# Performance work log

Hardware: AMD Instinct MI355X
Metric: run time of the kernel (lower is better)

## Reference

```python
import jax, jax.numpy as jnp
import numpy as np

F = 128          # nbr_fea_len
A = 64           # angle_fea_len
N_EDGES = 100_000
N_ANGLES = 400_000
N_CRYST = 512
EPS = 1e-5
INV_SQRT_2 = 1.0 / 2.0 ** 0.5


def layer_norm(x, g, b):
    mu = jnp.mean(x, axis=-1, keepdims=True)
    var = jnp.var(x, axis=-1, keepdims=True)
    return (x - mu) * jax.lax.rsqrt(var + EPS) * g + b


def setup_inputs() -> dict:
    key = jax.random.key(0)
    ks = jax.random.split(key, 16)
    def lin(k, out_f, in_f):
        return (jax.random.normal(k, (out_f, in_f), jnp.float32) * (1.0 / np.sqrt(in_f))).astype(jnp.float32)
    return {
        "nbr_fea": jax.random.normal(ks[0], (N_EDGES, F), jnp.float32),
        "angle_fea": jax.random.normal(ks[1], (N_ANGLES, A), jnp.float32),
        "angle_nbr_idx": jax.random.randint(ks[2], (N_ANGLES, 2), 0, N_EDGES),
        "crystal_edge_idx": jax.random.randint(ks[3], (N_EDGES,), 0, N_CRYST),
        "crystal_angle_index": jnp.sort(jax.random.randint(ks[4], (N_ANGLES,), 0, N_CRYST)),
        "W_full": lin(ks[5], 2 * F, 2 * F + A),
        "W_mask": lin(ks[6], 1, F),
        "cn_gamma": jnp.ones((2 * F,), jnp.float32),
        "cn_beta": jnp.zeros((2 * F,), jnp.float32),
        "ln_core_g": jnp.ones((F,), jnp.float32),
        "ln_core_b": jnp.zeros((F,), jnp.float32),
        "ln2_g": jnp.ones((F,), jnp.float32),
        "ln2_b": jnp.zeros((F,), jnp.float32),
        "res_W1a": lin(ks[7], F // 2, F), "res_b1a": jnp.zeros((F // 2,), jnp.float32),
        "res_W2a": lin(ks[8], F, F // 2), "res_b2a": jnp.zeros((F,), jnp.float32),
        "res_W1b": lin(ks[9], F // 2, F), "res_b1b": jnp.zeros((F // 2,), jnp.float32),
        "res_W2b": lin(ks[10], F, F // 2), "res_b2b": jnp.zeros((F,), jnp.float32),
    }


def reference(nbr_fea, angle_fea, angle_nbr_idx, crystal_edge_idx, crystal_angle_index,
              W_full, W_mask, cn_gamma, cn_beta, ln_core_g, ln_core_b, ln2_g, ln2_b,
              res_W1a, res_b1a, res_W2a, res_b2a, res_W1b, res_b1b, res_W2b, res_b2b):
    source_idx = angle_nbr_idx[:, 0]
    # gather the two neighbor edge features per angle -> [n_angles, 2F]
    pair = nbr_fea[angle_nbr_idx].reshape(-1, 2 * F)
    total = jnp.concatenate([angle_fea, pair], axis=1)          # [n_angles, 2F+A]
    h = total @ W_full.T                                        # [n_angles, 2F]

    # Crystal_Norm: per-crystal, per-feature normalization over angle rows
    seg = crystal_angle_index
    cnt = jnp.maximum(jax.ops.segment_sum(jnp.ones((h.shape[0], 1), h.dtype), seg, N_CRYST), 1.0)
    mean = jax.ops.segment_sum(h, seg, N_CRYST) / cnt
    diff = h - mean[seg]
    var = jax.ops.segment_sum(diff * diff, seg, N_CRYST) / cnt
    h = diff * jax.lax.rsqrt(var + EPS)[seg] * cn_gamma + cn_beta

    nbr_core, nbr_filter = h[:, :F], h[:, F:]
    nbr_core = jax.nn.silu(layer_norm(nbr_core, ln_core_g, ln_core_b))
    gate = jax.nn.sigmoid(nbr_filter @ W_mask.T)                # [n_angles, 1]
    msg = gate * nbr_core

    # scatter-mean over source edge; empty edges get 0 (matches scatter+pad)
    s = jax.ops.segment_sum(msg, source_idx, N_EDGES)
    c = jax.ops.segment_sum(jnp.ones((msg.shape[0], 1), msg.dtype), source_idx, N_EDGES)
    nbr_sumed = s / jnp.maximum(c, 1.0)

    x = layer_norm(nbr_sumed, ln2_g, ln2_b)
    # two residual bottleneck blocks: x + fc2(silu(fc1(x)))
    x = x + (jax.nn.silu(x @ res_W1a.T + res_b1a) @ res_W2a.T + res_b2a)
    x = x + (jax.nn.silu(x @ res_W1b.T + res_b1b) @ res_W2b.T + res_b2b)
    return INV_SQRT_2 * (nbr_fea + x)
```

## Files before the change

kernel.cpp:

```cpp
#include <hip/hip_runtime.h>
#include <hip/hip_bf16.h>
#include <hip/hip_fp16.h>
#include <cstdint>
#include <cstddef>

#define NF 128
#define N_EDGES 100000
#define N_ANGLES 400000
#define N_CRYST 512
#define KDIM 320
#define TWOF 256
#define EPS_LN 1e-5f
#define INV_SQRT_2 0.70710678118654752440f
#define CAP 32

typedef short short8 __attribute__((ext_vector_type(8)));
typedef float floatx4 __attribute__((ext_vector_type(4)));

__device__ inline unsigned short f2bf(float x) {
    __hip_bfloat16 b = __float2bfloat16(x);
    return *reinterpret_cast<unsigned short*>(&b);
}
__device__ inline float bf2f(__hip_bfloat16 b) { return __bfloat162float(b); }
__device__ inline float bfbits2f(unsigned short u) {
    unsigned int v = ((unsigned int)u) << 16;
    return __uint_as_float(v);
}

__device__ inline uint4 cvt8(float4 a, float4 b) {
    __hip_bfloat162 p0 = __float22bfloat162_rn(make_float2(a.x, a.y));
    __hip_bfloat162 p1 = __float22bfloat162_rn(make_float2(a.z, a.w));
    __hip_bfloat162 p2 = __float22bfloat162_rn(make_float2(b.x, b.y));
    __hip_bfloat162 p3 = __float22bfloat162_rn(make_float2(b.z, b.w));
    uint4 r;
    r.x = *reinterpret_cast<unsigned int*>(&p0);
    r.y = *reinterpret_cast<unsigned int*>(&p1);
    r.z = *reinterpret_cast<unsigned int*>(&p2);
    r.w = *reinterpret_cast<unsigned int*>(&p3);
    return r;
}

__global__ void seg_bounds(const int* __restrict__ seg, int* __restrict__ seg_start) {
    int s = blockIdx.x * blockDim.x + threadIdx.x;
    if (s > N_CRYST) return;
    if (s == N_CRYST) { seg_start[N_CRYST] = N_ANGLES; return; }
    int lo = 0, hi = N_ANGLES;
    while (lo < hi) { int mid = (lo + hi) >> 1; if (seg[mid] < s) lo = mid + 1; else hi = mid; }
    seg_start[s] = lo;
}

__global__ __launch_bounds__(512) void gemm_gather_mfma(
    const float* __restrict__ angle_fea,
    const float* __restrict__ nbr_fea,
    const int*   __restrict__ angle_nbr_idx,
    const float* __restrict__ W_full,
    __hip_bfloat16* __restrict__ hout)
{
    __shared__ uint4 X_lds[512];
    __shared__ uint4 W_lds[1024];

    const int tid  = threadIdx.x;
    const int row0 = blockIdx.x * 128;

    const int xm = tid >> 2;
    const int xk = ((tid & 3) ^ ((xm >> 1) & 3)) * 8;
    const int p0 = angle_nbr_idx[(size_t)(row0 + xm) * 2 + 0];
    const int p1 = angle_nbr_idx[(size_t)(row0 + xm) * 2 + 1];
    int wn[2], wk[2];
    #pragma unroll
    for (int it = 0; it < 2; ++it) {
        int tau = it * 512 + tid;
        wn[it] = tau >> 2;
        wk[it] = ((tau & 3) ^ ((wn[it] >> 1) & 3)) * 8;
    }

    const int wave = tid >> 6, lane = tid & 63;
    const int wrow = (wave & 1) * 64;
    const int wcol = (wave >> 1) * 64;
    const int rl   = lane & 15, kgrp = lane >> 4;
    const int fragoff = (kgrp ^ ((rl >> 1) & 3)) * 16;
    const char* Xb = (const char*)X_lds;
    const char* Wb = (const char*)W_lds;

    floatx4 acc[4][4];
    #pragma unroll
    for (int i = 0; i < 4; ++i)
        #pragma unroll
        for (int j = 0; j < 4; ++j)
            acc[i][j] = (floatx4){0.f, 0.f, 0.f, 0.f};

    float4 xa, xb2, wa0, wb0, wa1, wb1;
    auto loadX = [&](int kbase, float4& a, float4& b) {
        const float* src;
        if (kbase < 64)       src = angle_fea + (size_t)(row0 + xm) * 64 + kbase + xk;
        else if (kbase < 192) src = nbr_fea + (size_t)p0 * 128 + (kbase - 64) + xk;
        else                  src = nbr_fea + (size_t)p1 * 128 + (kbase - 192) + xk;
        a = ((const float4*)src)[0];
        b = ((const float4*)src)[1];
    };
    auto loadW = [&](int kbase, int it, float4& a, float4& b) {
        const float* src = W_full + (size_t)wn[it] * KDIM + kbase + wk[it];
        a = ((const float4*)src)[0];
        b = ((const float4*)src)[1];
    };

    loadX(0, xa, xb2);
    loadW(0, 0, wa0, wb0);
    loadW(0, 1, wa1, wb1);

    #pragma unroll
    for (int kiter = 0; kiter < 10; ++kiter) {
        uint4 xc  = cvt8(xa, xb2);
        uint4 wc0 = cvt8(wa0, wb0);
        uint4 wc1 = cvt8(wa1, wb1);
        if (kiter > 0) __syncthreads();
        X_lds[tid]       = xc;
        W_lds[tid]       = wc0;
        W_lds[512 + tid] = wc1;
        __syncthreads();
        if (kiter < 9) {
            int nb = (kiter + 1) * 32;
            loadX(nb, xa, xb2);
            loadW(nb, 0, wa0, wb0);
            loadW(nb, 1, wa1, wb1);
        }
        short8 wf[4], xf[4];
        #pragma unroll
        for (int i = 0; i < 4; ++i)
            wf[i] = *(const short8*)(Wb + (size_t)(wcol + i * 16 + rl) * 64 + fragoff);
        #pragma unroll
        for (int j = 0; j < 4; ++j)
            xf[j] = *(const short8*)(Xb + (size_t)(wrow + j * 16 + rl) * 64 + fragoff);
        #pragma unroll
        for (int i = 0; i < 4; ++i)
            #pragma unroll
            for (int j = 0; j < 4; ++j)
                acc[i][j] = __builtin_amdgcn_mfma_f32_16x16x32_bf16(wf[i], xf[j], acc[i][j], 0, 0, 0);
    }

    unsigned short* hp = reinterpret_cast<unsigned short*>(hout);
    #pragma unroll
    for (int j = 0; j < 4; ++j) {
        size_t r = (size_t)(row0 + wrow + j * 16 + rl);
        #pragma unroll
        for (int i = 0; i < 4; ++i) {
            int c = wcol + i * 16 + kgrp * 4;
            floatx4 v = acc[i][j];
            uint2 pk;
            pk.x = (unsigned int)f2bf(v[0]) | ((unsigned int)f2bf(v[1]) << 16);
            pk.y = (unsigned int)f2bf(v[2]) | ((unsigned int)f2bf(v[3]) << 16);
            *reinterpret_cast<uint2*>(hp + r * TWOF + c) = pk;
        }
    }
}

__global__ __launch_bounds__(256) void seg_stats(
    const __hip_bfloat16* __restrict__ h,
    const int* __restrict__ seg_start,
    float* __restrict__ segSum, float* __restrict__ segSumSq)
{
    __shared__ float redS[8][256];
    __shared__ float redQ[8][256];
    int seg   = blockIdx.x;
    int split = blockIdx.y;
    int start = seg_start[seg], end = seg_start[seg + 1];
    int n = end - start;
    int g = threadIdx.x >> 5, t = threadIdx.x & 31;
    float s[8] = {0.f,0.f,0.f,0.f,0.f,0.f,0.f,0.f};
    float q[8] = {0.f,0.f,0.f,0.f,0.f,0.f,0.f,0.f};
    if (n > 0) {
        int per = (n + 3) >> 2;
        int r0 = start + split * per;
        int r1 = min(r0 + per, end);
        const unsigned short* hp = (const unsigned short*)h;
        for (int r = r0 + g; r < r1; r += 8) {
            uint4 v = *(const uint4*)(hp + (size_t)r * TWOF + t * 8);
            unsigned int d[4] = {v.x, v.y, v.z, v.w};
            #pragma unroll
            for (int i = 0; i < 4; ++i) {
                float lo = __uint_as_float(d[i] << 16);
                float hi = __uint_as_float(d[i] & 0xffff0000u);
                s[2*i]   += lo; q[2*i]   += lo * lo;
                s[2*i+1] += hi; q[2*i+1] += hi * hi;
            }
        }
    }
    #pragma unroll
    for (int i = 0; i < 8; ++i) { redS[g][t * 8 + i] = s[i]; redQ[g][t * 8 + i] = q[i]; }
    __syncthreads();
    if (n > 0) {
        int col = threadIdx.x;
        float S = 0.f, Q = 0.f;
        #pragma unroll
        for (int gg = 0; gg < 8; ++gg) { S += redS[gg][col]; Q += redQ[gg][col]; }
        atomicAdd(&segSum[seg * TWOF + col], S);
        atomicAdd(&segSumSq[seg * TWOF + col], Q);
    }
}

__global__ __launch_bounds__(256) void seg_finalize(
    const int* __restrict__ seg_start,
    float* __restrict__ segSum, float* __restrict__ segSumSq)
{
    int seg = blockIdx.x;
    int j = threadIdx.x;
    float cnt = (float)max(seg_start[seg + 1] - seg_start[seg], 1);
    float inv = 1.0f / cnt;
    float mean = segSum[seg * TWOF + j] * inv;
    float var  = segSumSq[seg * TWOF + j] * inv - mean * mean;
    segSum[seg * TWOF + j]   = mean;
    segSumSq[seg * TWOF + j] = rsqrtf(var + EPS_LN);
}

__global__ __launch_bounds__(256) void angle_msg(
    __hip_bfloat16* __restrict__ h,
    const int* __restrict__ seg_idx,
    const int* __restrict__ angle_nbr_idx,
    const float* __restrict__ segMean, const float* __restrict__ segScale,
    const float* __restrict__ cn_gamma, const float* __restrict__ cn_beta,
    const float* __restrict__ ln_g, const float* __restrict__ ln_b,
    const float* __restrict__ w_mask,
    int* __restrict__ slot_cnt, int* __restrict__ slots)
{
    int row  = blockIdx.x * 4 + (threadIdx.x >> 6);
    int lane = threadIdx.x & 63;
    int seg  = seg_idx[row];
    int src  = angle_nbr_idx[(size_t)row * 2];

    __hip_bfloat16* hr = h + (size_t)row * TWOF;
    float y[4];
    #pragma unroll
    for (int qq = 0; qq < 4; ++qq) {
        int col = lane + qq * 64;
        float v = bf2f(hr[col]);
        float m = segMean[seg * TWOF + col], sc = segScale[seg * TWOF + col];
        y[qq] = (v - m) * sc * cn_gamma[col] + cn_beta[col];
    }
    float sum = y[0] + y[1], ssq = y[0] * y[0] + y[1] * y[1];
    #pragma unroll
    for (int o = 32; o > 0; o >>= 1) { sum += __shfl_xor(sum, o, 64); ssq += __shfl_xor(ssq, o, 64); }
    float mu  = sum * (1.f / 128.f);
    float var = ssq * (1.f / 128.f) - mu * mu;
    float rs  = rsqrtf(var + EPS_LN);
    float ln0 = (y[0] - mu) * rs * ln_g[lane]      + ln_b[lane];
    float ln1 = (y[1] - mu) * rs * ln_g[lane + 64] + ln_b[lane + 64];
    float si0 = ln0 / (1.f + __expf(-ln0));
    float si1 = ln1 / (1.f + __expf(-ln1));
    float gp = y[2] * w_mask[lane] + y[3] * w_mask[lane + 64];
    #pragma unroll
    for (int o = 32; o > 0; o >>= 1) gp += __shfl_xor(gp, o, 64);
    float gate = 1.f / (1.f + __expf(-gp));

    __half* mrow = reinterpret_cast<__half*>(hr);
    mrow[lane]      = __float2half(gate * si0);
    mrow[lane + 64] = __float2half(gate * si1);

    if (lane == 0) {
        int k = atomicAdd(&slot_cnt[src], 1);
        if (k < CAP) slots[(size_t)src * CAP + k] = row;
    }
}

#define MT 64
#define XBS 136
#define H1S 72
#define W1S 136
#define W2S 72
__global__ __launch_bounds__(256) void edge_mlp_mfma(
    const __hip_bfloat16* __restrict__ hmsg,
    const int* __restrict__ slot_cnt,
    const int* __restrict__ slots,
    const float* __restrict__ nbr_fea,
    const float* __restrict__ ln2_g, const float* __restrict__ ln2_b,
    const float* __restrict__ W1a, const float* __restrict__ b1a,
    const float* __restrict__ W2a, const float* __restrict__ b2a,
    const float* __restrict__ W1b, const float* __restrict__ b1b,
    const float* __restrict__ W2b, const float* __restrict__ b2b,
    float* __restrict__ out)
{
    __shared__ unsigned short xb[MT * XBS];
    __shared__ unsigned short h1[MT * H1S];
    __shared__ unsigned short wl[128 * W2S];

    const int tid  = threadIdx.x;
    const int row0 = blockIdx.x * MT;
    const int w    = tid >> 6, lane = tid & 63;
    const int rl   = lane & 15, kgrp = lane >> 4;

    {
        int m = tid >> 2;
        int q = tid & 3;
        int e = min(row0 + m, N_EDGES - 1);
        int cnt = min(slot_cnt[e], CAP);
        float v[32];
        #pragma unroll
        for (int i = 0; i < 32; ++i) v[i] = 0.f;
        const char* hb = (const char*)hmsg;
        for (int k = 0; k < cnt; ++k) {
            int r = slots[(size_t)e * CAP + k];
            const uint4* mr = (const uint4*)(hb + (size_t)r * 512 + q * 64);
            #pragma unroll
            for (int t = 0; t < 4; ++t) {
                uint4 u = mr[t];
                unsigned int d[4] = {u.x, u.y, u.z, u.w};
                #pragma unroll
                for (int i2 = 0; i2 < 4; ++i2) {
                    __half2 hh = *reinterpret_cast<__half2*>(&d[i2]);
                    float2 f2 = __half22float2(hh);
                    v[8*t + 2*i2]     += f2.x;
                    v[8*t + 2*i2 + 1] += f2.y;
                }
            }
        }
        float inv = 1.f / fmaxf((float)cnt, 1.f);
        float sum = 0.f, ssq = 0.f;
        #pragma unroll
        for (int i = 0; i < 32; ++i) { v[i] *= inv; sum += v[i]; ssq += v[i] * v[i]; }
        sum += __shfl_xor(sum, 1, 64); ssq += __shfl_xor(ssq, 1, 64);
        sum += __shfl_xor(sum, 2, 64); ssq += __shfl_xor(ssq, 2, 64);
        float mu  = sum * (1.f / 128.f);
        float var = ssq * (1.f / 128.f) - mu * mu;
        float rs  = rsqrtf(var + EPS_LN);
        #pragma unroll
        for (int i = 0; i < 32; ++i) {
            int col = q * 32 + i;
            v[i] = (v[i] - mu) * rs * ln2_g[col] + ln2_b[col];
        }
        #pragma unroll
        for (int t = 0; t < 4; ++t) {
            float4 a = make_float4(v[8*t+0], v[8*t+1], v[8*t+2], v[8*t+3]);
            float4 b = make_float4(v[8*t+4], v[8*t+5], v[8*t+6], v[8*t+7]);
            *(uint4*)&xb[m * XBS + q * 32 + t * 8] = cvt8(a, b);
        }
    }

    const float* W1s[2] = {W1a, W1b};
    const float* B1s[2] = {b1a, b1b};
    const float* W2s[2] = {W2a, W2b};
    const float* B2s[2] = {b2a, b2b};

    #pragma unroll 1
    for (int blk = 0; blk < 2; ++blk) {
        const float* W1 = W1s[blk]; const float* B1 = B1s[blk];
        const float* W2 = W2s[blk]; const float* B2 = B2s[blk];

        __syncthreads();
        #pragma unroll
        for (int c = tid; c < 1024; c += 256) {
            int nn = c >> 4, kc = c & 15;
            const float* src = W1 + (size_t)nn * 128 + kc * 8;
            *(uint4*)&wl[nn * W1S + kc * 8] =
                cvt8(((const float4*)src)[0], ((const float4*)src)[1]);
        }
        __syncthreads();

        short8 xf[4];
        #pragma unroll
        for (int ks = 0; ks < 4; ++ks)
            xf[ks] = *(const short8*)&xb[(w * 16 + rl) * XBS + ks * 32 + kgrp * 8];
        floatx4 a1[4];
        #pragma unroll
        for (int i = 0; i < 4; ++i) {
            a1[i] = (floatx4){0.f, 0.f, 0.f, 0.f};
            #pragma unroll
            for (int ks = 0; ks < 4; ++ks) {
                short8 wf = *(const short8*)&wl[(i * 16 + rl) * W1S + ks * 32 + kgrp * 8];
                a1[i] = __builtin_amdgcn_mfma_f32_16x16x32_bf16(wf, xf[ks], a1[i], 0, 0, 0);
            }
        }
        #pragma unroll
        for (int i = 0; i < 4; ++i) {
            int nb = i * 16 + kgrp * 4;
            float s0 = a1[i][0] + B1[nb + 0];
            float s1 = a1[i][1] + B1[nb + 1];
            float s2 = a1[i][2] + B1[nb + 2];
            float s3 = a1[i][3] + B1[nb + 3];
            s0 = s0 / (1.f + __expf(-s0));
            s1 = s1 / (1.f + __expf(-s1));
            s2 = s2 / (1.f + __expf(-s2));
            s3 = s3 / (1.f + __expf(-s3));
            unsigned int lo = (unsigned int)f2bf(s0) | ((unsigned int)f2bf(s1) << 16);
            unsigned int hi = (unsigned int)f2bf(s2) | ((unsigned int)f2bf(s3) << 16);
            *(unsigned int*)&h1[(w * 16 + rl) * H1S + nb]     = lo;
            *(unsigned int*)&h1[(w * 16 + rl) * H1S + nb + 2] = hi;
        }

        __syncthreads();
        #pragma unroll
        for (int c = tid; c < 1024; c += 256) {
            int pp = c >> 3, kc = c & 7;
            const float* src = W2 + (size_t)pp * 64 + kc * 8;
            *(uint4*)&wl[pp * W2S + kc * 8] =
                cvt8(((const float4*)src)[0], ((const float4*)src)[1]);
        }
        __syncthreads();

        short8 hf[2];
        #pragma unroll
        for (int ks = 0; ks < 2; ++ks)
            hf[ks] = *(const short8*)&h1[(w * 16 + rl) * H1S + ks * 32 + kgrp * 8];
        #pragma unroll
        for (int p = 0; p < 8; ++p) {
            floatx4 a2 = (floatx4){0.f, 0.f, 0.f, 0.f};
            #pragma unroll
            for (int ks = 0; ks < 2; ++ks) {
                short8 wf = *(const short8*)&wl[(p * 16 + rl) * W2S + ks * 32 + kgrp * 8];
                a2 = __builtin_amdgcn_mfma_f32_16x16x32_bf16(wf, hf[ks], a2, 0, 0, 0);
            }
            int m = w * 16 + rl;
            #pragma unroll
            for (int reg = 0; reg < 4; ++reg) {
                int pcol = p * 16 + kgrp * 4 + reg;
                int idx  = m * XBS + pcol;
                float xv = bfbits2f(xb[idx]);
                xb[idx] = f2bf(xv + a2[reg] + B2[pcol]);
            }
        }
    }

    {
        int m = tid >> 2;
        int q = tid & 3;
        int e = row0 + m;
        if (e < N_EDGES) {
            const float4* nf = (const float4*)(nbr_fea + (size_t)e * NF + q * 32);
            float4* dst      = (float4*)(out + (size_t)e * NF + q * 32);
            #pragma unroll
            for (int t = 0; t < 8; ++t) {
                float4 f = nf[t];
                int col = q * 32 + 4 * t;
                dst[t] = make_float4(
                    INV_SQRT_2 * (f.x + bfbits2f(xb[m * XBS + col + 0])),
                    INV_SQRT_2 * (f.y + bfbits2f(xb[m * XBS + col + 1])),
                    INV_SQRT_2 * (f.z + bfbits2f(xb[m * XBS + col + 2])),
                    INV_SQRT_2 * (f.w + bfbits2f(xb[m * XBS + col + 3])));
            }
        }
    }
}


extern "C" void kernel_launch(void* const* d_in, const int* in_sizes, int n_in,
                              void* d_out, int out_size, void* d_ws, size_t ws_size,
                              hipStream_t stream) {
    const float* nbr_fea       = (const float*)d_in[0];
    const float* angle_fea     = (const float*)d_in[1];
    const int*   angle_nbr_idx = (const int*)d_in[2];
    const int*   cai           = (const int*)d_in[4];
    const float* W_full        = (const float*)d_in[5];
    const float* W_mask        = (const float*)d_in[6];
    const float* cn_gamma      = (const float*)d_in[7];
    const float* cn_beta       = (const float*)d_in[8];
    const float* ln_core_g     = (const float*)d_in[9];
    const float* ln_core_b     = (const float*)d_in[10];
    const float* ln2_g         = (const float*)d_in[11];
    const float* ln2_b         = (const float*)d_in[12];
    const float* W1a           = (const float*)d_in[13];
    const float* b1a           = (const float*)d_in[14];
    const float* W2a           = (const float*)d_in[15];
    const float* b2a           = (const float*)d_in[16];
    const float* W1b           = (const float*)d_in[17];
    const float* b1b           = (const float*)d_in[18];
    const float* W2b           = (const float*)d_in[19];
    const float* b2b           = (const float*)d_in[20];
    float* out = (float*)d_out;

    char* ws = (char*)d_ws;
    float* segSum    = (float*)(ws + 0);
    float* segSumSq  = (float*)(ws + 524288);
    int*   slot_cnt  = (int*)  (ws + 1048576);
    int*   seg_start = (int*)  (ws + 1448576);
    int*   slots     = (int*)  (ws + 1450752);
    __hip_bfloat16* h = (__hip_bfloat16*)(ws + 14250752);

    hipMemsetAsync(ws, 0, 1448576, stream);

    seg_bounds<<<3, 256, 0, stream>>>(cai, seg_start);
    gemm_gather_mfma<<<N_ANGLES / 128, 512, 0, stream>>>(
        angle_fea, nbr_fea, angle_nbr_idx, W_full, h);
    seg_stats<<<dim3(N_CRYST, 4), 256, 0, stream>>>(h, seg_start, segSum, segSumSq);
    seg_finalize<<<N_CRYST, 256, 0, stream>>>(seg_start, segSum, segSumSq);
    angle_msg<<<N_ANGLES / 4, 256, 0, stream>>>(
        h, cai, angle_nbr_idx, segSum, segSumSq,
        cn_gamma, cn_beta, ln_core_g, ln_core_b, W_mask, slot_cnt, slots);
    edge_mlp_mfma<<<(N_EDGES + MT - 1) / MT, 256, 0, stream>>>(
        h, slot_cnt, slots, nbr_fea, ln2_g, ln2_b,
        W1a, b1a, W2a, b2a, W1b, b1b, W2b, b2b, out);
}
```

Measured before the change: 666.1 us.

## Fuse segment statistics into GEMM epilogue and double-buffer GEMM LDS

After: 718.9 us. 1.08x slower.

```diff
diff --git a/kernel.cpp b/kernel.cpp
--- a/kernel.cpp
+++ b/kernel.cpp
@@ -54,10 +54,12 @@
     const float* __restrict__ nbr_fea,
     const int*   __restrict__ angle_nbr_idx,
     const float* __restrict__ W_full,
+    const int*   __restrict__ cai,
+    float* __restrict__ segSum, float* __restrict__ segSumSq,
     __hip_bfloat16* __restrict__ hout)
 {
-    __shared__ uint4 X_lds[512];
-    __shared__ uint4 W_lds[1024];
+    __shared__ uint4 X_lds[2][512];
+    __shared__ uint4 W_lds[2][1024];
 
     const int tid  = threadIdx.x;
     const int row0 = blockIdx.x * 128;
@@ -79,8 +81,6 @@
     const int wcol = (wave >> 1) * 64;
     const int rl   = lane & 15, kgrp = lane >> 4;
     const int fragoff = (kgrp ^ ((rl >> 1) & 3)) * 16;
-    const char* Xb = (const char*)X_lds;
-    const char* Wb = (const char*)W_lds;
 
     floatx4 acc[4][4];
     #pragma unroll
@@ -89,41 +89,44 @@
         for (int j = 0; j < 4; ++j)
             acc[i][j] = (floatx4){0.f, 0.f, 0.f, 0.f};
 
-    float4 xa, xb2, wa0, wb0, wa1, wb1;
-    auto loadX = [&](int kbase, float4& a, float4& b) {
+    float4 xr[2][2];
+    float4 wr[2][4];
+    auto loadX = [&](int kbase, int s) {
         const float* src;
         if (kbase < 64)       src = angle_fea + (size_t)(row0 + xm) * 64 + kbase + xk;
         else if (kbase < 192) src = nbr_fea + (size_t)p0 * 128 + (kbase - 64) + xk;
         else                  src = nbr_fea + (size_t)p1 * 128 + (kbase - 192) + xk;
-        a = ((const float4*)src)[0];
-        b = ((const float4*)src)[1];
+        xr[s][0] = ((const float4*)src)[0];
+        xr[s][1] = ((const float4*)src)[1];
     };
-    auto loadW = [&](int kbase, int it, float4& a, float4& b) {
-        const float* src = W_full + (size_t)wn[it] * KDIM + kbase + wk[it];
-        a = ((const float4*)src)[0];
-        b = ((const float4*)src)[1];
+    auto loadW = [&](int kbase, int s) {
+        const float* s0 = W_full + (size_t)wn[0] * KDIM + kbase + wk[0];
+        wr[s][0] = ((const float4*)s0)[0];
+        wr[s][1] = ((const float4*)s0)[1];
+        const float* s1 = W_full + (size_t)wn[1] * KDIM + kbase + wk[1];
+        wr[s][2] = ((const float4*)s1)[0];
+        wr[s][3] = ((const float4*)s1)[1];
     };
 
-    loadX(0, xa, xb2);
-    loadW(0, 0, wa0, wb0);
-    loadW(0, 1, wa1, wb1);
-
-    #pragma unroll
-    for (int kiter = 0; kiter < 10; ++kiter) {
-        uint4 xc  = cvt8(xa, xb2);
-        uint4 wc0 = cvt8(wa0, wb0);
-        uint4 wc1 = cvt8(wa1, wb1);
-        if (kiter > 0) __syncthreads();
-        X_lds[tid]       = xc;
-        W_lds[tid]       = wc0;
-        W_lds[512 + tid] = wc1;
-        __syncthreads();
-        if (kiter < 9) {
-            int nb = (kiter + 1) * 32;
-            loadX(nb, xa, xb2);
-            loadW(nb, 0, wa0, wb0);
-            loadW(nb, 1, wa1, wb1);
-        }
+    loadX(0, 0);  loadW(0, 0);
+    loadX(32, 1); loadW(32, 1);
+    {
+        uint4 xc  = cvt8(xr[0][0], xr[0][1]);
+        uint4 wc0 = cvt8(wr[0][0], wr[0][1]);
+        uint4 wc1 = cvt8(wr[0][2], wr[0][3]);
+        X_lds[0][tid]       = xc;
+        W_lds[0][tid]       = wc0;
+        W_lds[0][512 + tid] = wc1;
+    }
+    loadX(64, 0); loadW(64, 0);
+    asm volatile("s_waitcnt lgkmcnt(0)" ::: "memory");
+    __builtin_amdgcn_s_barrier();
+
+    #pragma unroll
+    for (int k = 0; k < 10; ++k) {
+        const int cur = k & 1, nxt = (k + 1) & 1;
+        const char* Xb = (const char*)X_lds[cur];
+        const char* Wb = (const char*)W_lds[cur];
         short8 wf[4], xf[4];
         #pragma unroll
         for (int i = 0; i < 4; ++i)
@@ -131,11 +134,27 @@
         #pragma unroll
         for (int j = 0; j < 4; ++j)
             xf[j] = *(const short8*)(Xb + (size_t)(wrow + j * 16 + rl) * 64 + fragoff);
+        if (k < 9) {
+            uint4 xc  = cvt8(xr[nxt][0], xr[nxt][1]);
+            uint4 wc0 = cvt8(wr[nxt][0], wr[nxt][1]);
+            uint4 wc1 = cvt8(wr[nxt][2], wr[nxt][3]);
+            X_lds[nxt][tid]       = xc;
+            W_lds[nxt][tid]       = wc0;
+            W_lds[nxt][512 + tid] = wc1;
+            if (k + 3 <= 9) {
+                loadX((k + 3) * 32, nxt);
+                loadW((k + 3) * 32, nxt);
+            }
+        }
         #pragma unroll
         for (int i = 0; i < 4; ++i)
             #pragma unroll
             for (int j = 0; j < 4; ++j)
                 acc[i][j] = __builtin_amdgcn_mfma_f32_16x16x32_bf16(wf[i], xf[j], acc[i][j], 0, 0, 0);
+        if (k < 9) {
+            asm volatile("s_waitcnt lgkmcnt(0)" ::: "memory");
+            __builtin_amdgcn_s_barrier();
+        }
     }
 
     unsigned short* hp = reinterpret_cast<unsigned short*>(hout);
@@ -152,49 +171,55 @@
             *reinterpret_cast<uint2*>(hp + r * TWOF + c) = pk;
         }
     }
-}
-
-__global__ __launch_bounds__(256) void seg_stats(
-    const __hip_bfloat16* __restrict__ h,
-    const int* __restrict__ seg_start,
-    float* __restrict__ segSum, float* __restrict__ segSumSq)
-{
-    __shared__ float redS[8][256];
-    __shared__ float redQ[8][256];
-    int seg   = blockIdx.x;
-    int split = blockIdx.y;
-    int start = seg_start[seg], end = seg_start[seg + 1];
-    int n = end - start;
-    int g = threadIdx.x >> 5, t = threadIdx.x & 31;
-    float s[8] = {0.f,0.f,0.f,0.f,0.f,0.f,0.f,0.f};
-    float q[8] = {0.f,0.f,0.f,0.f,0.f,0.f,0.f,0.f};
-    if (n > 0) {
-        int per = (n + 3) >> 2;
-        int r0 = start + split * per;
-        int r1 = min(r0 + per, end);
-        const unsigned short* hp = (const unsigned short*)h;
-        for (int r = r0 + g; r < r1; r += 8) {
-            uint4 v = *(const uint4*)(hp + (size_t)r * TWOF + t * 8);
-            unsigned int d[4] = {v.x, v.y, v.z, v.w};
-            #pragma unroll
-            for (int i = 0; i < 4; ++i) {
-                float lo = __uint_as_float(d[i] << 16);
-                float hi = __uint_as_float(d[i] & 0xffff0000u);
-                s[2*i]   += lo; q[2*i]   += lo * lo;
-                s[2*i+1] += hi; q[2*i+1] += hi * hi;
-            }
-        }
-    }
-    #pragma unroll
-    for (int i = 0; i < 8; ++i) { redS[g][t * 8 + i] = s[i]; redQ[g][t * 8 + i] = q[i]; }
-    __syncthreads();
-    if (n > 0) {
-        int col = threadIdx.x;
-        float S = 0.f, Q = 0.f;
-        #pragma unroll
-        for (int gg = 0; gg < 8; ++gg) { S += redS[gg][col]; Q += redQ[gg][col]; }
-        atomicAdd(&segSum[seg * TWOF + col], S);
-        atomicAdd(&segSumSq[seg * TWOF + col], Q);
+
+    float* red = (float*)&X_lds[0][0];
+    int sj[4];
+    #pragma unroll
+    for (int j = 0; j < 4; ++j) sj[j] = cai[row0 + wrow + j * 16 + rl];
+    const int sA = cai[row0], sB = cai[row0 + 127];
+    for (int s = sA; s <= sB; ++s) {
+        float S[16], Q[16];
+        #pragma unroll
+        for (int t = 0; t < 16; ++t) { S[t] = 0.f; Q[t] = 0.f; }
+        #pragma unroll
+        for (int j = 0; j < 4; ++j) {
+            float msk = (sj[j] == s) ? 1.f : 0.f;
+            #pragma unroll
+            for (int i = 0; i < 4; ++i)
+                #pragma unroll
+                for (int g = 0; g < 4; ++g) {
+                    float v = acc[i][j][g] * msk;
+                    S[i * 4 + g] += v;
+                    Q[i * 4 + g] += v * v;
+                }
+        }
+        #pragma unroll
+        for (int t = 0; t < 16; ++t) {
+            #pragma unroll
+            for (int d = 1; d < 16; d <<= 1) {
+                S[t] += __shfl_xor(S[t], d, 64);
+                Q[t] += __shfl_xor(Q[t], d, 64);
+            }
+        }
+        __syncthreads();
+        if (rl == 0) {
+            #pragma unroll
+            for (int i = 0; i < 4; ++i)
+                #pragma unroll
+                for (int g = 0; g < 4; ++g) {
+                    int col = wcol + i * 16 + kgrp * 4 + g;
+                    red[((wave & 1) * 256 + col) * 2 + 0] = S[i * 4 + g];
+                    red[((wave & 1) * 256 + col) * 2 + 1] = Q[i * 4 + g];
+                }
+        }
+        __syncthreads();
+        if (tid < 256) {
+            int col = tid;
+            float Ss = red[col * 2]     + red[(256 + col) * 2];
+            float Qs = red[col * 2 + 1] + red[(256 + col) * 2 + 1];
+            atomicAdd(&segSum[(size_t)s * TWOF + col], Ss);
+            atomicAdd(&segSumSq[(size_t)s * TWOF + col], Qs);
+        }
     }
 }
 
@@ -227,33 +252,45 @@
     int seg  = seg_idx[row];
     int src  = angle_nbr_idx[(size_t)row * 2];
 
-    __hip_bfloat16* hr = h + (size_t)row * TWOF;
-    float y[4];
-    #pragma unroll
-    for (int qq = 0; qq < 4; ++qq) {
-        int col = lane + qq * 64;
-        float v = bf2f(hr[col]);
-        float m = segMean[seg * TWOF + col], sc = segScale[seg * TWOF + col];
-        y[qq] = (v - m) * sc * cn_gamma[col] + cn_beta[col];
-    }
-    float sum = y[0] + y[1], ssq = y[0] * y[0] + y[1] * y[1];
+    unsigned short* hr = reinterpret_cast<unsigned short*>(h + (size_t)row * TWOF);
+    const int c0 = 2 * lane;
+    unsigned int ucore = ((const unsigned int*)hr)[lane];
+    unsigned int ufilt = ((const unsigned int*)hr)[lane + 64];
+
+    float2 m0 = *(const float2*)&segMean[seg * TWOF + c0];
+    float2 s0 = *(const float2*)&segScale[seg * TWOF + c0];
+    float2 m1 = *(const float2*)&segMean[seg * TWOF + 128 + c0];
+    float2 s1 = *(const float2*)&segScale[seg * TWOF + 128 + c0];
+    float2 g0 = *(const float2*)&cn_gamma[c0];
+    float2 b0 = *(const float2*)&cn_beta[c0];
+    float2 g1 = *(const float2*)&cn_gamma[128 + c0];
+    float2 b1 = *(const float2*)&cn_beta[128 + c0];
+
+    float y0 = (bfbits2f((unsigned short)(ucore & 0xffffu)) - m0.x) * s0.x * g0.x + b0.x;
+    float y1 = (bfbits2f((unsigned short)(ucore >> 16))     - m0.y) * s0.y * g0.y + b0.y;
+    float y2 = (bfbits2f((unsigned short)(ufilt & 0xffffu)) - m1.x) * s1.x * g1.x + b1.x;
+    float y3 = (bfbits2f((unsigned short)(ufilt >> 16))     - m1.y) * s1.y * g1.y + b1.y;
+
+    float sum = y0 + y1, ssq = y0 * y0 + y1 * y1;
     #pragma unroll
     for (int o = 32; o > 0; o >>= 1) { sum += __shfl_xor(sum, o, 64); ssq += __shfl_xor(ssq, o, 64); }
     float mu  = sum * (1.f / 128.f);
     float var = ssq * (1.f / 128.f) - mu * mu;
     float rs  = rsqrtf(var + EPS_LN);
-    float ln0 = (y[0] - mu) * rs * ln_g[lane]      + ln_b[lane];
-    float ln1 = (y[1] - mu) * rs * ln_g[lane + 64] + ln_b[lane + 64];
+    float2 lg = *(const float2*)&ln_g[c0];
+    float2 lb = *(const float2*)&ln_b[c0];
+    float ln0 = (y0 - mu) * rs * lg.x + lb.x;
+    float ln1 = (y1 - mu) * rs * lg.y + lb.y;
     float si0 = ln0 / (1.f + __expf(-ln0));
     float si1 = ln1 / (1.f + __expf(-ln1));
-    float gp = y[2] * w_mask[lane] + y[3] * w_mask[lane + 64];
+    float2 wm = *(const float2*)&w_mask[c0];
+    float gp = y2 * wm.x + y3 * wm.y;
     #pragma unroll
     for (int o = 32; o > 0; o >>= 1) gp += __shfl_xor(gp, o, 64);
     float gate = 1.f / (1.f + __expf(-gp));
 
-    __half* mrow = reinterpret_cast<__half*>(hr);
-    mrow[lane]      = __float2half(gate * si0);
-    mrow[lane + 64] = __float2half(gate * si1);
+    __half2 hh = __floats2half2_rn(gate * si0, gate * si1);
+    ((unsigned int*)hr)[lane] = *reinterpret_cast<unsigned int*>(&hh);
 
     if (lane == 0) {
         int k = atomicAdd(&slot_cnt[src], 1);
@@ -477,8 +514,7 @@
 
     seg_bounds<<<3, 256, 0, stream>>>(cai, seg_start);
     gemm_gather_mfma<<<N_ANGLES / 128, 512, 0, stream>>>(
-        angle_fea, nbr_fea, angle_nbr_idx, W_full, h);
-    seg_stats<<<dim3(N_CRYST, 4), 256, 0, stream>>>(h, seg_start, segSum, segSumSq);
+        angle_fea, nbr_fea, angle_nbr_idx, W_full, cai, segSum, segSumSq, h);
     seg_finalize<<<N_CRYST, 256, 0, stream>>>(seg_start, segSum, segSumSq);
     angle_msg<<<N_ANGLES / 4, 256, 0, stream>>>(
         h, cai, angle_nbr_idx, segSum, segSumSq,
```

## Fuse per-crystal sum and sum-of-squares into the gather GEMM epilogue

Applied to the files above, without the earlier changes.

After: 750.2 us. 12.6% more time.

```diff
diff --git a/kernel.cpp b/kernel.cpp
--- a/kernel.cpp
+++ b/kernel.cpp
@@ -54,10 +54,13 @@
     const float* __restrict__ nbr_fea,
     const int*   __restrict__ angle_nbr_idx,
     const float* __restrict__ W_full,
+    const int*   __restrict__ cai,
+    float* __restrict__ segSum, float* __restrict__ segSumSq,
     __hip_bfloat16* __restrict__ hout)
 {
     __shared__ uint4 X_lds[512];
     __shared__ uint4 W_lds[1024];
+    __shared__ float red[1024];
 
     const int tid  = threadIdx.x;
     const int row0 = blockIdx.x * 128;
@@ -152,49 +155,43 @@
             *reinterpret_cast<uint2*>(hp + r * TWOF + c) = pk;
         }
     }
-}
-
-__global__ __launch_bounds__(256) void seg_stats(
-    const __hip_bfloat16* __restrict__ h,
-    const int* __restrict__ seg_start,
-    float* __restrict__ segSum, float* __restrict__ segSumSq)
-{
-    __shared__ float redS[8][256];
-    __shared__ float redQ[8][256];
-    int seg   = blockIdx.x;
-    int split = blockIdx.y;
-    int start = seg_start[seg], end = seg_start[seg + 1];
-    int n = end - start;
-    int g = threadIdx.x >> 5, t = threadIdx.x & 31;
-    float s[8] = {0.f,0.f,0.f,0.f,0.f,0.f,0.f,0.f};
-    float q[8] = {0.f,0.f,0.f,0.f,0.f,0.f,0.f,0.f};
-    if (n > 0) {
-        int per = (n + 3) >> 2;
-        int r0 = start + split * per;
-        int r1 = min(r0 + per, end);
-        const unsigned short* hp = (const unsigned short*)h;
-        for (int r = r0 + g; r < r1; r += 8) {
-            uint4 v = *(const uint4*)(hp + (size_t)r * TWOF + t * 8);
-            unsigned int d[4] = {v.x, v.y, v.z, v.w};
-            #pragma unroll
-            for (int i = 0; i < 4; ++i) {
-                float lo = __uint_as_float(d[i] << 16);
-                float hi = __uint_as_float(d[i] & 0xffff0000u);
-                s[2*i]   += lo; q[2*i]   += lo * lo;
-                s[2*i+1] += hi; q[2*i+1] += hi * hi;
-            }
-        }
-    }
-    #pragma unroll
-    for (int i = 0; i < 8; ++i) { redS[g][t * 8 + i] = s[i]; redQ[g][t * 8 + i] = q[i]; }
-    __syncthreads();
-    if (n > 0) {
-        int col = threadIdx.x;
-        float S = 0.f, Q = 0.f;
-        #pragma unroll
-        for (int gg = 0; gg < 8; ++gg) { S += redS[gg][col]; Q += redQ[gg][col]; }
-        atomicAdd(&segSum[seg * TWOF + col], S);
-        atomicAdd(&segSumSq[seg * TWOF + col], Q);
+
+    int sj[4];
+    #pragma unroll
+    for (int j = 0; j < 4; ++j) sj[j] = cai[row0 + wrow + j * 16 + rl];
+    const int sA = cai[row0], sB = cai[row0 + 127];
+    for (int s = sA; s <= sB; ++s) {
+        __syncthreads();
+        #pragma unroll
+        for (int i = 0; i < 4; ++i) {
+            #pragma unroll
+            for (int g = 0; g < 4; ++g) {
+                float S = 0.f, Q = 0.f;
+                #pragma unroll
+                for (int j = 0; j < 4; ++j) {
+                    float v = (sj[j] == s) ? acc[i][j][g] : 0.f;
+                    S += v;
+                    Q += v * v;
+                }
+                S += __shfl_xor(S, 1, 64); Q += __shfl_xor(Q, 1, 64);
+                S += __shfl_xor(S, 2, 64); Q += __shfl_xor(Q, 2, 64);
+                S += __shfl_xor(S, 4, 64); Q += __shfl_xor(Q, 4, 64);
+                S += __shfl_xor(S, 8, 64); Q += __shfl_xor(Q, 8, 64);
+                if (rl == 0) {
+                    int col = wcol + i * 16 + kgrp * 4 + g;
+                    red[((wave & 1) * 256 + col) * 2 + 0] = S;
+                    red[((wave & 1) * 256 + col) * 2 + 1] = Q;
+                }
+            }
+        }
+        __syncthreads();
+        if (tid < 256) {
+            int col = tid;
+            float Ss = red[col * 2]     + red[(256 + col) * 2];
+            float Qs = red[col * 2 + 1] + red[(256 + col) * 2 + 1];
+            atomicAdd(&segSum[(size_t)s * TWOF + col], Ss);
+            atomicAdd(&segSumSq[(size_t)s * TWOF + col], Qs);
+        }
     }
 }
 
@@ -477,8 +474,7 @@
 
     seg_bounds<<<3, 256, 0, stream>>>(cai, seg_start);
     gemm_gather_mfma<<<N_ANGLES / 128, 512, 0, stream>>>(
-        angle_fea, nbr_fea, angle_nbr_idx, W_full, h);
-    seg_stats<<<dim3(N_CRYST, 4), 256, 0, stream>>>(h, seg_start, segSum, segSumSq);
+        angle_fea, nbr_fea, angle_nbr_idx, W_full, cai, segSum, segSumSq, h);
     seg_finalize<<<N_CRYST, 256, 0, stream>>>(seg_start, segSum, segSumSq);
     angle_msg<<<N_ANGLES / 4, 256, 0, stream>>>(
         h, cai, angle_nbr_idx, segSum, segSumSq,
```

## Fuse per-angle message computation into edge MLP gather, precompute affine norm

Applied to the files above, without the earlier changes.

Measured after the change: 826.2 us. +24.0%, slower.

```diff
diff --git a/kernel.cpp b/kernel.cpp
--- a/kernel.cpp
+++ b/kernel.cpp
@@ -47,6 +47,17 @@
     int lo = 0, hi = N_ANGLES;
     while (lo < hi) { int mid = (lo + hi) >> 1; if (seg[mid] < s) lo = mid + 1; else hi = mid; }
     seg_start[s] = lo;
+}
+
+__global__ __launch_bounds__(256) void slot_build(
+    const int* __restrict__ angle_nbr_idx,
+    int* __restrict__ slot_cnt, int* __restrict__ slots)
+{
+    int row = blockIdx.x * 256 + threadIdx.x;
+    if (row >= N_ANGLES) return;
+    int src = angle_nbr_idx[(size_t)row * 2];
+    int k = atomicAdd(&slot_cnt[src], 1);
+    if (k < CAP) slots[(size_t)src * CAP + k] = row;
 }
 
 __global__ __launch_bounds__(512) void gemm_gather_mfma(
@@ -200,6 +211,7 @@
 
 __global__ __launch_bounds__(256) void seg_finalize(
     const int* __restrict__ seg_start,
+    const float* __restrict__ cn_gamma, const float* __restrict__ cn_beta,
     float* __restrict__ segSum, float* __restrict__ segSumSq)
 {
     int seg = blockIdx.x;
@@ -208,57 +220,11 @@
     float inv = 1.0f / cnt;
     float mean = segSum[seg * TWOF + j] * inv;
     float var  = segSumSq[seg * TWOF + j] * inv - mean * mean;
-    segSum[seg * TWOF + j]   = mean;
-    segSumSq[seg * TWOF + j] = rsqrtf(var + EPS_LN);
-}
-
-__global__ __launch_bounds__(256) void angle_msg(
-    __hip_bfloat16* __restrict__ h,
-    const int* __restrict__ seg_idx,
-    const int* __restrict__ angle_nbr_idx,
-    const float* __restrict__ segMean, const float* __restrict__ segScale,
-    const float* __restrict__ cn_gamma, const float* __restrict__ cn_beta,
-    const float* __restrict__ ln_g, const float* __restrict__ ln_b,
-    const float* __restrict__ w_mask,
-    int* __restrict__ slot_cnt, int* __restrict__ slots)
-{
-    int row  = blockIdx.x * 4 + (threadIdx.x >> 6);
-    int lane = threadIdx.x & 63;
-    int seg  = seg_idx[row];
-    int src  = angle_nbr_idx[(size_t)row * 2];
-
-    __hip_bfloat16* hr = h + (size_t)row * TWOF;
-    float y[4];
-    #pragma unroll
-    for (int qq = 0; qq < 4; ++qq) {
-        int col = lane + qq * 64;
-        float v = bf2f(hr[col]);
-        float m = segMean[seg * TWOF + col], sc = segScale[seg * TWOF + col];
-        y[qq] = (v - m) * sc * cn_gamma[col] + cn_beta[col];
-    }
-    float sum = y[0] + y[1], ssq = y[0] * y[0] + y[1] * y[1];
-    #pragma unroll
-    for (int o = 32; o > 0; o >>= 1) { sum += __shfl_xor(sum, o, 64); ssq += __shfl_xor(ssq, o, 64); }
-    float mu  = sum * (1.f / 128.f);
-    float var = ssq * (1.f / 128.f) - mu * mu;
-    float rs  = rsqrtf(var + EPS_LN);
-    float ln0 = (y[0] - mu) * rs * ln_g[lane]      + ln_b[lane];
-    float ln1 = (y[1] - mu) * rs * ln_g[lane + 64] + ln_b[lane + 64];
-    float si0 = ln0 / (1.f + __expf(-ln0));
-    float si1 = ln1 / (1.f + __expf(-ln1));
-    float gp = y[2] * w_mask[lane] + y[3] * w_mask[lane + 64];
-    #pragma unroll
-    for (int o = 32; o > 0; o >>= 1) gp += __shfl_xor(gp, o, 64);
-    float gate = 1.f / (1.f + __expf(-gp));
-
-    __half* mrow = reinterpret_cast<__half*>(hr);
-    mrow[lane]      = __float2half(gate * si0);
-    mrow[lane + 64] = __float2half(gate * si1);
-
-    if (lane == 0) {
-        int k = atomicAdd(&slot_cnt[src], 1);
-        if (k < CAP) slots[(size_t)src * CAP + k] = row;
-    }
+    float rs   = rsqrtf(var + EPS_LN);
+    float A = rs * cn_gamma[j];
+    float B = cn_beta[j] - mean * A;
+    segSum[seg * TWOF + j]   = A;
+    segSumSq[seg * TWOF + j] = B;
 }
 
 #define MT 64
@@ -267,10 +233,14 @@
 #define W1S 136
 #define W2S 72
 __global__ __launch_bounds__(256) void edge_mlp_mfma(
-    const __hip_bfloat16* __restrict__ hmsg,
+    const __hip_bfloat16* __restrict__ h,
+    const int* __restrict__ cai,
     const int* __restrict__ slot_cnt,
     const int* __restrict__ slots,
+    const float* __restrict__ segA, const float* __restrict__ segB,
     const float* __restrict__ nbr_fea,
+    const float* __restrict__ lncg, const float* __restrict__ lncb,
+    const float* __restrict__ w_mask,
     const float* __restrict__ ln2_g, const float* __restrict__ ln2_b,
     const float* __restrict__ W1a, const float* __restrict__ b1a,
     const float* __restrict__ W2a, const float* __restrict__ b2a,
@@ -281,41 +251,100 @@
     __shared__ unsigned short xb[MT * XBS];
     __shared__ unsigned short h1[MT * H1S];
     __shared__ unsigned short wl[128 * W2S];
+    __shared__ float lnw[384];
 
     const int tid  = threadIdx.x;
     const int row0 = blockIdx.x * MT;
     const int w    = tid >> 6, lane = tid & 63;
     const int rl   = lane & 15, kgrp = lane >> 4;
+
+    if (tid < 128) {
+        lnw[tid]       = lncg[tid];
+        lnw[128 + tid] = lncb[tid];
+        lnw[256 + tid] = w_mask[tid];
+    }
+    __syncthreads();
 
     {
         int m = tid >> 2;
         int q = tid & 3;
         int e = min(row0 + m, N_EDGES - 1);
         int cnt = min(slot_cnt[e], CAP);
-        float v[32];
-        #pragma unroll
-        for (int i = 0; i < 32; ++i) v[i] = 0.f;
-        const char* hb = (const char*)hmsg;
+        float acc[32];
+        #pragma unroll
+        for (int i = 0; i < 32; ++i) acc[i] = 0.f;
+        const char* hb = (const char*)h;
+
         for (int k = 0; k < cnt; ++k) {
-            int r = slots[(size_t)e * CAP + k];
-            const uint4* mr = (const uint4*)(hb + (size_t)r * 512 + q * 64);
+            int r   = slots[(size_t)e * CAP + k];
+            int seg = cai[r];
+            const uint4* hrow = (const uint4*)(hb + (size_t)r * 512);
+            const float* Asg = segA + (size_t)seg * TWOF;
+            const float* Bsg = segB + (size_t)seg * TWOF;
+
+            float y[32];
+            float sum = 0.f, ssq = 0.f, gp = 0.f;
             #pragma unroll
             for (int t = 0; t < 4; ++t) {
-                uint4 u = mr[t];
-                unsigned int d[4] = {u.x, u.y, u.z, u.w};
+                uint4 u = hrow[q * 4 + t];
+                float A8[8], B8[8];
+                *(float4*)&A8[0] = *(const float4*)(Asg + q * 32 + t * 8);
+                *(float4*)&A8[4] = *(const float4*)(Asg + q * 32 + t * 8 + 4);
+                *(float4*)&B8[0] = *(const float4*)(Bsg + q * 32 + t * 8);
+                *(float4*)&B8[4] = *(const float4*)(Bsg + q * 32 + t * 8 + 4);
+                unsigned int dd[4] = {u.x, u.y, u.z, u.w};
                 #pragma unroll
-                for (int i2 = 0; i2 < 4; ++i2) {
-                    __half2 hh = *reinterpret_cast<__half2*>(&d[i2]);
-                    float2 f2 = __half22float2(hh);
-                    v[8*t + 2*i2]     += f2.x;
-                    v[8*t + 2*i2 + 1] += f2.y;
+                for (int j = 0; j < 4; ++j) {
+                    float lo = bfbits2f((unsigned short)(dd[j] & 0xffffu));
+                    float hi = bfbits2f((unsigned short)(dd[j] >> 16));
+                    float y0 = lo * A8[2*j]     + B8[2*j];
+                    float y1 = hi * A8[2*j + 1] + B8[2*j + 1];
+                    y[t*8 + 2*j]     = y0;
+                    y[t*8 + 2*j + 1] = y1;
+                    sum += y0 + y1;
+                    ssq += y0 * y0 + y1 * y1;
                 }
             }
-        }
+            #pragma unroll
+            for (int t = 0; t < 4; ++t) {
+                uint4 u = hrow[16 + q * 4 + t];
+                float A8[8], B8[8];
+                *(float4*)&A8[0] = *(const float4*)(Asg + 128 + q * 32 + t * 8);
+                *(float4*)&A8[4] = *(const float4*)(Asg + 128 + q * 32 + t * 8 + 4);
+                *(float4*)&B8[0] = *(const float4*)(Bsg + 128 + q * 32 + t * 8);
+                *(float4*)&B8[4] = *(const float4*)(Bsg + 128 + q * 32 + t * 8 + 4);
+                unsigned int dd[4] = {u.x, u.y, u.z, u.w};
+                #pragma unroll
+                for (int j = 0; j < 4; ++j) {
+                    float lo = bfbits2f((unsigned short)(dd[j] & 0xffffu));
+                    float hi = bfbits2f((unsigned short)(dd[j] >> 16));
+                    float y0 = lo * A8[2*j]     + B8[2*j];
+                    float y1 = hi * A8[2*j + 1] + B8[2*j + 1];
+                    gp += y0 * lnw[256 + q * 32 + t * 8 + 2*j];
+                    gp += y1 * lnw[256 + q * 32 + t * 8 + 2*j + 1];
+                }
+            }
+            sum += __shfl_xor(sum, 1, 64); ssq += __shfl_xor(ssq, 1, 64); gp += __shfl_xor(gp, 1, 64);
+            sum += __shfl_xor(sum, 2, 64); ssq += __shfl_xor(ssq, 2, 64); gp += __shfl_xor(gp, 2, 64);
+            float mu  = sum * (1.f / 128.f);
+            float var = ssq * (1.f / 128.f) - mu * mu;
+            float rs  = rsqrtf(var + EPS_LN);
+            float gate = 1.f / (1.f + __expf(-gp));
+            #pragma unroll
+            for (int i = 0; i < 32; ++i) {
+                float ln = (y[i] - mu) * rs * lnw[q * 32 + i] + lnw[128 + q * 32 + i];
+                acc[i] += gate * (ln / (1.f + __expf(-ln)));
+            }
+        }
+
         float inv = 1.f / fmaxf((float)cnt, 1.f);
         float sum = 0.f, ssq = 0.f;
         #pragma unroll
-        for (int i = 0; i < 32; ++i) { v[i] *= inv; sum += v[i]; ssq += v[i] * v[i]; }
+        for (int i = 0; i < 32; ++i) {
+            acc[i] *= inv;
+            sum += acc[i];
+            ssq += acc[i] * acc[i];
+        }
         sum += __shfl_xor(sum, 1, 64); ssq += __shfl_xor(ssq, 1, 64);
         sum += __shfl_xor(sum, 2, 64); ssq += __shfl_xor(ssq, 2, 64);
         float mu  = sum * (1.f / 128.f);
@@ -324,12 +353,12 @@
         #pragma unroll
         for (int i = 0; i < 32; ++i) {
             int col = q * 32 + i;
-            v[i] = (v[i] - mu) * rs * ln2_g[col] + ln2_b[col];
+            acc[i] = (acc[i] - mu) * rs * ln2_g[col] + ln2_b[col];
         }
         #pragma unroll
         for (int t = 0; t < 4; ++t) {
-            float4 a = make_float4(v[8*t+0], v[8*t+1], v[8*t+2], v[8*t+3]);
-            float4 b = make_float4(v[8*t+4], v[8*t+5], v[8*t+6], v[8*t+7]);
+            float4 a = make_float4(acc[8*t+0], acc[8*t+1], acc[8*t+2], acc[8*t+3]);
+            float4 b = make_float4(acc[8*t+4], acc[8*t+5], acc[8*t+6], acc[8*t+7]);
             *(uint4*)&xb[m * XBS + q * 32 + t * 8] = cvt8(a, b);
         }
     }
@@ -476,14 +505,13 @@
     hipMemsetAsync(ws, 0, 1448576, stream);
 
     seg_bounds<<<3, 256, 0, stream>>>(cai, seg_start);
+    slot_build<<<(N_ANGLES + 255) / 256, 256, 0, stream>>>(angle_nbr_idx, slot_cnt, slots);
     gemm_gather_mfma<<<N_ANGLES / 128, 512, 0, stream>>>(
         angle_fea, nbr_fea, angle_nbr_idx, W_full, h);
     seg_stats<<<dim3(N_CRYST, 4), 256, 0, stream>>>(h, seg_start, segSum, segSumSq);
-    seg_finalize<<<N_CRYST, 256, 0, stream>>>(seg_start, segSum, segSumSq);
-    angle_msg<<<N_ANGLES / 4, 256, 0, stream>>>(
-        h, cai, angle_nbr_idx, segSum, segSumSq,
-        cn_gamma, cn_beta, ln_core_g, ln_core_b, W_mask, slot_cnt, slots);
+    seg_finalize<<<N_CRYST, 256, 0, stream>>>(seg_start, cn_gamma, cn_beta, segSum, segSumSq);
     edge_mlp_mfma<<<(N_EDGES + MT - 1) / MT, 256, 0, stream>>>(
-        h, slot_cnt, slots, nbr_fea, ln2_g, ln2_b,
+        h, cai, slot_cnt, slots, segSum, segSumSq, nbr_fea,
+        ln_core_g, ln_core_b, W_mask, ln2_g, ln2_b,
         W1a, b1a, W2a, b2a, W1b, b1b, W2b, b2b, out);
 }
```
